# Optimization experiments

Measured on AMD Instinct MI355X. Metric: run time of the kernel, lower is better.

The kernel has to match this reference:

```python
import jax, jax.numpy as jnp
import numpy as np

B, N, DIM = 4, 2048, 3
H = 128          # hidden
K = 32           # num_neighbours
L = 4            # num_layers
OUT = 6          # out_per_particle


def _dense_init(key, fan_in, fan_out):
    kw, kb = jax.random.split(key)
    w = jax.random.normal(kw, (fan_in, fan_out), jnp.float32) / np.sqrt(fan_in)
    b = jnp.zeros((fan_out,), jnp.float32)
    return w, b


def setup_inputs() -> dict:
    key = jax.random.key(0)
    ks = jax.random.split(key, 8)
    x = jax.random.normal(ks[0], (B, N, DIM), jnp.float32)
    embed_w, embed_b = _dense_init(ks[1], DIM, H)
    # per-layer stacked params
    miw, mib, mow, mob, uiw, uib, uow, uob = [], [], [], [], [], [], [], []
    for l in range(L):
        k0, k1, k2, k3 = jax.random.split(jax.random.fold_in(ks[2], l), 4)
        w, b = _dense_init(k0, 2 * H + 1, H); miw.append(w); mib.append(b)
        w, b = _dense_init(k1, H, H);         mow.append(w); mob.append(b)
        w, b = _dense_init(k2, 2 * H, H);     uiw.append(w); uib.append(b)
        w, b = _dense_init(k3, H, H);         uow.append(w); uob.append(b)
    out_w, out_b = _dense_init(ks[3], H, OUT)
    return {
        'x': x,
        'embed_w': embed_w, 'embed_b': embed_b,
        'msg_in_w': jnp.stack(miw), 'msg_in_b': jnp.stack(mib),
        'msg_out_w': jnp.stack(mow), 'msg_out_b': jnp.stack(mob),
        'upd_in_w': jnp.stack(uiw), 'upd_in_b': jnp.stack(uib),
        'upd_out_w': jnp.stack(uow), 'upd_out_b': jnp.stack(uob),
        'out_w': out_w, 'out_b': out_b,
    }


def reference(x, embed_w, embed_b,
              msg_in_w, msg_in_b, msg_out_w, msg_out_b,
              upd_in_w, upd_in_b, upd_out_w, upd_out_b,
              out_w, out_b):
    act = jax.nn.silu
    n = x.shape[-2]
    # per-particle embed: (B,N,H)
    h = x @ embed_w + embed_b
    # pairwise squared distances (B,N,N), plain Euclidean (geometry=None)
    diff = x[..., :, None, :] - x[..., None, :, :]
    d_sq = jnp.sum(diff * diff, axis=-1)
    eye = jnp.eye(n, dtype=bool)
    d_sq = jnp.where(eye, jnp.inf, d_sq)
    neg_topk, idx_topk = jax.lax.top_k(-d_sq, K)      # (B,N,K)
    d_nearest = jnp.sqrt(jnp.maximum(-neg_topk, 0.0))  # (B,N,K)

    gather = jax.vmap(lambda hb, ib: hb[ib])  # (N,H),(N,K)->(N,K,H) over batch
    n_layers = msg_in_w.shape[0]
    for l in range(n_layers):
        nb = gather(h, idx_topk)                               # (B,N,K,H)
        node_i = jnp.broadcast_to(h[..., :, None, :], nb.shape)
        msg_inp = jnp.concatenate([node_i, nb, d_nearest[..., None]], axis=-1)
        msg = act(msg_inp @ msg_in_w[l] + msg_in_b[l]) @ msg_out_w[l] + msg_out_b[l]
        agg = jnp.sum(msg, axis=-2)                            # (B,N,H)
        upd_inp = jnp.concatenate([h, agg], axis=-1)
        upd = act(upd_inp @ upd_in_w[l] + upd_in_b[l]) @ upd_out_w[l] + upd_out_b[l]
        h = h + upd
    return h @ out_w + out_b
```

## Files before the change

kernel.cpp:

```cpp
#include <hip/hip_runtime.h>
#include <math.h>

#define B_ 4
#define N_ 2048
#define H_ 128
#define K_ 32
#define L_ 4
#define OUT_ 6
#define BN_ (B_*N_)
#define NPB_L 16
#define LBLK 512

typedef __attribute__((ext_vector_type(8))) short short8;
typedef __attribute__((ext_vector_type(4))) float f32x4;

#define LDW (H_ + 8)
#define LAYER_W 98304
#define OFF_W1A 0
#define OFF_W1C 16384
#define OFF_W2  32768
#define OFF_U1  49152
#define OFF_U2  81920
#define SCAP 256
#define KNN_ROWS 4
#define KNN_BLKS (BN_/KNN_ROWS)
#define PREP_BLKS (L_*LAYER_W/256)

#define LOG2E 1.44269504088896340736f
#define LN2   0.69314718055994530942f

__device__ __forceinline__ float silu_f(float x) {
    return __fdividef(x, 1.0f + __expf(-x));
}
__device__ __forceinline__ float silu_y(float y) {
    return __fdividef(y, 1.0f + __builtin_amdgcn_exp2f(-y));
}
__device__ __forceinline__ short f2b(float f) {
    unsigned u = __float_as_uint(f);
    return (short)((u + 0x7FFFu + ((u >> 16) & 1u)) >> 16);
}
__device__ __forceinline__ float b2f(short s) {
    return __uint_as_float(((unsigned)(unsigned short)s) << 16);
}
__device__ __forceinline__ unsigned pack2(short lo, short hi) {
    return (unsigned)(unsigned short)lo | ((unsigned)(unsigned short)hi << 16);
}
__device__ __forceinline__ int mbcnt64(unsigned long long m) {
    return __builtin_amdgcn_mbcnt_hi((unsigned)(m >> 32),
           __builtin_amdgcn_mbcnt_lo((unsigned)m, 0));
}

__global__ __launch_bounds__(256) void k_front(
    const float* __restrict__ x, int* __restrict__ nidx, float* __restrict__ ndist,
    const float* __restrict__ miw, const float* __restrict__ mow,
    const float* __restrict__ uiw, const float* __restrict__ uow,
    short* __restrict__ wt,
    const float* __restrict__ ew, const float* __restrict__ eb,
    const float* __restrict__ mib, float* __restrict__ Epack)
{
    __shared__ float xsx[N_], xsy[N_], xsz[N_];
    __shared__ unsigned skey[KNN_ROWS][SCAP];
    __shared__ int      sid [KNN_ROWS][SCAP];

    if (blockIdx.x >= KNN_BLKS + PREP_BLKS) {
        int t = threadIdx.x;
        int which = t >> 7, n = t & 127;
        const float* W = miw + (size_t)(which ? 128 : 0) * H_;
        float E0 = 0.f, E1 = 0.f, E2 = 0.f, Eb = 0.f;
        for (int k = 0; k < 128; ++k) {
            float w = W[(size_t)k*H_ + n];
            E0 = fmaf(ew[k],       w, E0);
            E1 = fmaf(ew[128 + k], w, E1);
            E2 = fmaf(ew[256 + k], w, E2);
            Eb = fmaf(eb[k],       w, Eb);
        }
        float* dst = Epack + which * 512;
        dst[0*128 + n] = E0 * LOG2E;
        dst[1*128 + n] = E1 * LOG2E;
        dst[2*128 + n] = E2 * LOG2E;
        dst[3*128 + n] = (Eb + (which ? 0.f : mib[n])) * LOG2E;
        return;
    }
    if (blockIdx.x >= KNN_BLKS) {
        int gid = (blockIdx.x - KNN_BLKS) * 256 + threadIdx.x;
        int l = gid / LAYER_W, o = gid - l * LAYER_W;
        float v;
        if (o < OFF_W1C) {
            int n = o >> 7, k = o & 127;
            v = miw[(size_t)l*257*H_ + k*H_ + n] * LOG2E;
        } else if (o < OFF_W2) {
            int oo = o - OFF_W1C, n = oo >> 7, k = oo & 127;
            v = miw[(size_t)l*257*H_ + (128 + k)*H_ + n] * LOG2E;
        } else if (o < OFF_U1) {
            int oo = o - OFF_W2, n = oo >> 7, k = oo & 127;
            v = mow[(size_t)l*H_*H_ + k*H_ + n];
        } else if (o < OFF_U2) {
            int oo = o - OFF_U1, n = oo >> 8, k = oo & 255;
            v = uiw[(size_t)l*2*H_*H_ + k*H_ + n];
        } else {
            int oo = o - OFF_U2, n = oo >> 7, k = oo & 127;
            v = uow[(size_t)l*H_*H_ + k*H_ + n];
        }
        wt[gid] = f2b(v);
        return;
    }

    int b  = blockIdx.x / (N_/KNN_ROWS);
    int i0 = (blockIdx.x % (N_/KNN_ROWS)) * KNN_ROWS;
    const float* xb = x + (size_t)b*N_*3;
    for (int t = threadIdx.x; t < N_*3; t += 256) {
        float v = xb[t];
        int q = t / 3, r = t - q*3;
        float* dst = (r == 0) ? xsx : (r == 1) ? xsy : xsz;
        dst[q] = v;
    }
    __syncthreads();

    int wave = threadIdx.x >> 6, lane = threadIdx.x & 63;
    int i = i0 + wave;
    float xix = xsx[i], xiy = xsy[i], xiz = xsz[i];

    unsigned u[N_/64];
    unsigned lmin = 0xFFFFFFFFu;
#pragma unroll
    for (int t = 0; t < N_/64; ++t) {
        int j = lane + 64*t;
        float d0 = xix-xsx[j], d1 = xiy-xsy[j], d2 = xiz-xsz[j];
        float d = d0*d0 + d1*d1 + d2*d2;
        unsigned k = (j == i) ? 0x7F800000u : __float_as_uint(d);
        u[t] = k;
        lmin = min(lmin, k);
    }
    unsigned mn = lmin, mx = lmin;
    for (int off = 32; off; off >>= 1) {
        unsigned o1 = (unsigned)__shfl_xor((int)mn, off); mn = min(mn, o1);
        unsigned o2 = (unsigned)__shfl_xor((int)mx, off); mx = max(mx, o2);
    }
    unsigned Tup = mn;
    if (mn != mx) {
        int hb = 31 - __clz((int)(mn ^ mx));
        Tup = mn & ~((2u << hb) - 1u);
        for (int bit = hb; bit >= 0; --bit) {
            unsigned cand = Tup | (1u << bit);
            if (__popcll(__ballot(lmin < cand)) < K_) Tup = cand;
        }
    }
    unsigned* sk = skey[wave];
    int*      si = sid [wave];
    int base = 0;
#pragma unroll
    for (int t = 0; t < N_/64; ++t) {
        bool pr = (u[t] <= Tup);
        unsigned long long m = __ballot(pr);
        if (pr) {
            int pos = base + mbcnt64(m);
            if (pos < SCAP) { sk[pos] = u[t]; si[pos] = lane + 64*t; }
        }
        base += __popcll(m);
    }
    int c = min(base, SCAP);
    unsigned sv[4]; int iv[4];
#pragma unroll
    for (int q = 0; q < 4; ++q) {
        int slot = lane + 64*q;
        bool ok = slot < c;
        sv[q] = ok ? sk[slot] : 0xFFFFFFFFu;
        iv[q] = ok ? si[slot] : 0;
    }
    unsigned T = mn;
    if (mn != Tup) {
        int hb = 31 - __clz((int)(mn ^ Tup));
        T = mn & ~((2u << hb) - 1u);
        for (int bit = hb; bit >= 0; --bit) {
            unsigned cand = T | (1u << bit);
            int cnt = __popcll(__ballot(sv[0] < cand)) + __popcll(__ballot(sv[1] < cand))
                    + __popcll(__ballot(sv[2] < cand)) + __popcll(__ballot(sv[3] < cand));
            if (cnt < K_) T = cand;
        }
    }
    int cnt_lt = __popcll(__ballot(sv[0] < T)) + __popcll(__ballot(sv[1] < T))
               + __popcll(__ballot(sv[2] < T)) + __popcll(__ballot(sv[3] < T));
    int need = K_ - cnt_lt;
    size_t rbase = ((size_t)(b*N_ + i)) * K_;
    int ltc = 0, eqc = 0;
#pragma unroll
    for (int q = 0; q < 4; ++q) {
        bool lt = sv[q] < T, eq = sv[q] == T;
        unsigned long long mlt = __ballot(lt), meq = __ballot(eq);
        int pp = ltc + mbcnt64(mlt), ee = eqc + mbcnt64(meq);
        ltc += __popcll(mlt); eqc += __popcll(meq);
        int pos = lt ? pp : ((eq && ee < need) ? (cnt_lt + ee) : -1);
        if (pos >= 0) {
            nidx [rbase + pos] = iv[q];
            ndist[rbase + pos] = sqrtf(__uint_as_float(sv[q]));
        }
    }
}

__global__ __launch_bounds__(512) void k_prep0(
    float* __restrict__ h, short* __restrict__ a, short* __restrict__ c0,
    const float* __restrict__ x, const float* __restrict__ ew,
    const float* __restrict__ eb, const float* __restrict__ Epack)
{
    int t = blockIdx.x * 512 + threadIdx.x;
    int node = t >> 7, ch = t & 127;
    const float* xp = x + (size_t)node*3;
    float x0 = xp[0], x1 = xp[1], x2 = xp[2];
    float hv = eb[ch];
    hv = fmaf(x0, ew[ch],       hv);
    hv = fmaf(x1, ew[H_+ch],    hv);
    hv = fmaf(x2, ew[2*H_+ch],  hv);
    float av = Epack[384+ch];
    av = fmaf(x0, Epack[ch],     av);
    av = fmaf(x1, Epack[128+ch], av);
    av = fmaf(x2, Epack[256+ch], av);
    float cv = Epack[896+ch];
    cv = fmaf(x0, Epack[512+ch], cv);
    cv = fmaf(x1, Epack[640+ch], cv);
    cv = fmaf(x2, Epack[768+ch], cv);
    size_t gi = (size_t)node*H_ + ch;
    h[gi]  = hv;
    a[gi]  = f2b(av);
    c0[gi] = f2b(cv);
}

__global__ __launch_bounds__(LBLK, 4) void k_layer(
    float* __restrict__ h, short* __restrict__ a,
    const int* __restrict__ nidx, const float* __restrict__ ndist,
    const float* __restrict__ wd,
    const short* __restrict__ wl,
    const float* __restrict__ b2, const float* __restrict__ u1b,
    const float* __restrict__ u2b,
    const short* __restrict__ c_rd, short* __restrict__ c_wr,
    const short* __restrict__ wn, const float* __restrict__ b1n, int do_ac,
    const float* __restrict__ ow, const float* __restrict__ ob,
    float* __restrict__ out)
{
    __shared__ __align__(16) short s_l[NPB_L][LDW];
    __shared__ __align__(16) short h_l[NPB_L][LDW];
    __shared__ __align__(16) short agg_l[NPB_L][LDW];
    __shared__ __align__(16) float h32s[NPB_L][H_];
    __shared__ int   idx_s[NPB_L][K_];
    __shared__ float dst_s[NPB_L][K_];
    int blk = blockIdx.x;
    int batch = (blk & 7) >> 1;
    int sub   = ((blk >> 3) << 1) | (blk & 1);
    int node0 = batch * N_ + sub * NPB_L;
    int tid = threadIdx.x;
    int wave = tid >> 6, lane = tid & 63, l15 = lane & 15, quad = lane >> 4;
    int ncol = wave*16 + l15;

    {
        float4 v = reinterpret_cast<const float4*>(h + (size_t)node0*H_)[tid];
        int row = tid >> 5, col = (tid & 31) * 4;
        h_l[row][col+0] = f2b(v.x); h_l[row][col+1] = f2b(v.y);
        h_l[row][col+2] = f2b(v.z); h_l[row][col+3] = f2b(v.w);
        *(float4*)&h32s[row][col] = v;
    }
    idx_s[tid>>5][tid&31] = nidx[(size_t)node0*K_ + tid];
    dst_s[tid>>5][tid&31] = ndist[(size_t)node0*K_ + tid];
    __syncthreads();

    short8 bw2[4];
#pragma unroll
    for (int kk = 0; kk < 4; ++kk)
        bw2[kk] = *(const short8*)(wl + OFF_W2 + (size_t)ncol*H_ + kk*32 + quad*8);

    {
        float wd0 = wd[2*lane] * LOG2E, wd1 = wd[2*lane+1] * LOG2E;
        int wavu = __builtin_amdgcn_readfirstlane(wave);
        const unsigned* c2 = (const unsigned*)c_rd + (size_t)batch*N_*(H_/2);
        const unsigned* a2 = (const unsigned*)a;
        int m0 = wavu*2, m1 = wavu*2 + 1;
        unsigned av0 = a2[(size_t)(node0+m0)*(H_/2) + lane];
        unsigned av1 = a2[(size_t)(node0+m1)*(H_/2) + lane];
        unsigned cv0[K_], cv1[K_];
#pragma unroll
        for (int k = 0; k < K_; ++k) {
            int j = __builtin_amdgcn_readfirstlane(idx_s[m0][k]);
            cv0[k] = c2[(size_t)j*(H_/2) + lane];
        }
#pragma unroll
        for (int k = 0; k < K_; ++k) {
            int j = __builtin_amdgcn_readfirstlane(idx_s[m1][k]);
            cv1[k] = c2[(size_t)j*(H_/2) + lane];
        }
        {
            float a0 = __uint_as_float(av0 << 16);
            float a1 = __uint_as_float(av0 & 0xFFFF0000u);
            float s0 = 0.f, s1 = 0.f;
#pragma unroll
            for (int k = 0; k < K_; ++k) {
                float dd = dst_s[m0][k];
                s0 += silu_y(a0 + fmaf(dd, wd0, __uint_as_float(cv0[k] << 16)));
                s1 += silu_y(a1 + fmaf(dd, wd1, __uint_as_float(cv0[k] & 0xFFFF0000u)));
            }
            *(unsigned*)&s_l[m0][2*lane] = pack2(f2b(s0 * LN2), f2b(s1 * LN2));
        }
        {
            float a0 = __uint_as_float(av1 << 16);
            float a1 = __uint_as_float(av1 & 0xFFFF0000u);
            float s0 = 0.f, s1 = 0.f;
#pragma unroll
            for (int k = 0; k < K_; ++k) {
                float dd = dst_s[m1][k];
                s0 += silu_y(a0 + fmaf(dd, wd0, __uint_as_float(cv1[k] << 16)));
                s1 += silu_y(a1 + fmaf(dd, wd1, __uint_as_float(cv1[k] & 0xFFFF0000u)));
            }
            *(unsigned*)&s_l[m1][2*lane] = pack2(f2b(s0 * LN2), f2b(s1 * LN2));
        }
    }
    short8 bu1[8], bu2[4];
#pragma unroll
    for (int kk = 0; kk < 8; ++kk)
        bu1[kk] = *(const short8*)(wl + OFF_U1 + (size_t)ncol*2*H_ + kk*32 + quad*8);
#pragma unroll
    for (int kk = 0; kk < 4; ++kk)
        bu2[kk] = *(const short8*)(wl + OFF_U2 + (size_t)ncol*H_ + kk*32 + quad*8);
    __syncthreads();

    f32x4 acc;
    acc = (f32x4){0,0,0,0};
#pragma unroll
    for (int kk = 0; kk < 4; ++kk) {
        int k0 = kk*32 + quad*8;
        short8 af = *(const short8*)&s_l[l15][k0];
        acc = __builtin_amdgcn_mfma_f32_16x16x32_bf16(af, bw2[kk], acc, 0, 0, 0);
    }
    {
        float b2v = b2[ncol] * (float)K_;
#pragma unroll
        for (int r = 0; r < 4; ++r)
            agg_l[quad*4 + r][ncol] = f2b(acc[r] + b2v);
    }
    __syncthreads();

    acc = (f32x4){0,0,0,0};
#pragma unroll
    for (int kk = 0; kk < 8; ++kk) {
        const short (*src)[LDW] = (kk < 4) ? h_l : agg_l;
        int kloc = ((kk < 4) ? kk*32 : (kk-4)*32) + quad*8;
        short8 af = *(const short8*)&src[l15][kloc];
        acc = __builtin_amdgcn_mfma_f32_16x16x32_bf16(af, bu1[kk], acc, 0, 0, 0);
    }
    short8 bacA[4], bacC[4];
    if (do_ac) {
#pragma unroll
        for (int kk = 0; kk < 4; ++kk) {
            bacA[kk] = *(const short8*)(wn + OFF_W1A + (size_t)ncol*H_ + kk*32 + quad*8);
            bacC[kk] = *(const short8*)(wn + OFF_W1C + (size_t)ncol*H_ + kk*32 + quad*8);
        }
    }
    {
        float u1bv = u1b[ncol];
#pragma unroll
        for (int r = 0; r < 4; ++r)
            s_l[quad*4 + r][ncol] = f2b(silu_f(acc[r] + u1bv));
    }
    __syncthreads();

    acc = (f32x4){0,0,0,0};
#pragma unroll
    for (int kk = 0; kk < 4; ++kk) {
        int k0 = kk*32 + quad*8;
        short8 af = *(const short8*)&s_l[l15][k0];
        acc = __builtin_amdgcn_mfma_f32_16x16x32_bf16(af, bu2[kk], acc, 0, 0, 0);
    }
    {
        float u2bv = u2b[ncol];
#pragma unroll
        for (int r = 0; r < 4; ++r) {
            int m = quad*4 + r;
            float nh = h32s[m][ncol] + acc[r] + u2bv;
            h[(size_t)(node0+m)*H_ + ncol] = nh;
            if (do_ac) h_l[m][ncol] = f2b(nh);
            else       h32s[m][ncol] = nh;
        }
    }
    if (do_ac) {
        __syncthreads();
        int n = ncol;
        f32x4 accA = (f32x4){0,0,0,0}, accC = (f32x4){0,0,0,0};
#pragma unroll
        for (int kk = 0; kk < 4; ++kk) {
            int k0 = kk*32 + quad*8;
            short8 af = *(const short8*)&h_l[l15][k0];
            accA = __builtin_amdgcn_mfma_f32_16x16x32_bf16(af, bacA[kk], accA, 0, 0, 0);
            accC = __builtin_amdgcn_mfma_f32_16x16x32_bf16(af, bacC[kk], accC, 0, 0, 0);
        }
        float b1v = b1n[n] * LOG2E;
#pragma unroll
        for (int r = 0; r < 4; ++r) {
            int m = quad*4 + r;
            size_t gi = (size_t)(node0+m)*H_ + n;
            a[gi]    = f2b(accA[r] + b1v);
            c_wr[gi] = f2b(accC[r]);
        }
    } else {
        __syncthreads();
        int node = tid >> 5, s = tid & 31;
        float p0=0.f,p1=0.f,p2=0.f,p3=0.f,p4=0.f,p5=0.f;
#pragma unroll
        for (int q = 0; q < 4; ++q) {
            int r = s + q*32;
            float hv = h32s[node][r];
            const float* owr = ow + r*OUT_;
            p0 = fmaf(hv, owr[0], p0); p1 = fmaf(hv, owr[1], p1);
            p2 = fmaf(hv, owr[2], p2); p3 = fmaf(hv, owr[3], p3);
            p4 = fmaf(hv, owr[4], p4); p5 = fmaf(hv, owr[5], p5);
        }
#pragma unroll
        for (int off = 16; off; off >>= 1) {
            p0 += __shfl_xor(p0, off); p1 += __shfl_xor(p1, off);
            p2 += __shfl_xor(p2, off); p3 += __shfl_xor(p3, off);
            p4 += __shfl_xor(p4, off); p5 += __shfl_xor(p5, off);
        }
        if (s == 0) {
            float* op = out + (size_t)(node0+node)*OUT_;
            op[0] = p0 + ob[0]; op[1] = p1 + ob[1]; op[2] = p2 + ob[2];
            op[3] = p3 + ob[3]; op[4] = p4 + ob[4]; op[5] = p5 + ob[5];
        }
    }
}

extern "C" void kernel_launch(void* const* d_in, const int* in_sizes, int n_in,
                              void* d_out, int out_size, void* d_ws, size_t ws_size,
                              hipStream_t stream)
{
    const float* x   = (const float*)d_in[0];
    const float* ew  = (const float*)d_in[1];
    const float* eb  = (const float*)d_in[2];
    const float* miw = (const float*)d_in[3];
    const float* mib = (const float*)d_in[4];
    const float* mow = (const float*)d_in[5];
    const float* mob = (const float*)d_in[6];
    const float* uiw = (const float*)d_in[7];
    const float* uib = (const float*)d_in[8];
    const float* uow = (const float*)d_in[9];
    const float* uob = (const float*)d_in[10];
    const float* ow  = (const float*)d_in[11];
    const float* ob  = (const float*)d_in[12];
    float* out = (float*)d_out;

    char* w = (char*)d_ws;
    float* h  = (float*)w;                         w += (size_t)BN_*H_*4;
    float* nd = (float*)w;                         w += (size_t)BN_*K_*4;
    int*   ni = (int*)w;                           w += (size_t)BN_*K_*4;
    short* a  = (short*)w;                         w += (size_t)BN_*H_*2;
    short* c0 = (short*)w;                         w += (size_t)BN_*H_*2;
    short* c1 = (short*)w;                         w += (size_t)BN_*H_*2;
    short* wt = (short*)w;                         w += (size_t)L_*LAYER_W*2;
    float* Epack = (float*)w;

    k_front<<<KNN_BLKS + PREP_BLKS + 1, 256, 0, stream>>>(x, ni, nd,
        miw, mow, uiw, uow, wt, ew, eb, mib, Epack);
    k_prep0<<<BN_*H_/512, 512, 0, stream>>>(h, a, c0, x, ew, eb, Epack);
    for (int l = 0; l < L_; ++l) {
        const short* c_rd = (l & 1) ? c1 : c0;
        short*       c_wr = (l & 1) ? c0 : c1;
        int do_ac = (l + 1 < L_);
        const short* wn = wt + (size_t)(do_ac ? (l+1) : l) * LAYER_W;
        const float* b1n = mib + (size_t)(do_ac ? (l+1) : l) * H_;
        k_layer<<<BN_/NPB_L, LBLK, 0, stream>>>(h, a, ni, nd,
            miw + (size_t)l*257*H_ + 256*H_,
            wt + (size_t)l*LAYER_W,
            mob + (size_t)l*H_, uib + (size_t)l*H_, uob + (size_t)l*H_,
            c_rd, c_wr, wn, b1n, do_ac,
            ow, ob, out);
    }
}
```

Baseline: 224.8 us.

## Fuse prep and per-layer kernels into one persistent kernel with grid barriers

Result: slower. 403.3 us (+79.4%).

```diff
diff --git a/kernel.cpp b/kernel.cpp
--- a/kernel.cpp
+++ b/kernel.cpp
@@ -10,6 +10,7 @@
 #define BN_ (B_*N_)
 #define NPB_L 16
 #define LBLK 512
+#define MAIN_BLKS (BN_/NPB_L)
 
 typedef __attribute__((ext_vector_type(8))) short short8;
 typedef __attribute__((ext_vector_type(4))) float f32x4;
@@ -39,15 +40,23 @@
     unsigned u = __float_as_uint(f);
     return (short)((u + 0x7FFFu + ((u >> 16) & 1u)) >> 16);
 }
-__device__ __forceinline__ float b2f(short s) {
-    return __uint_as_float(((unsigned)(unsigned short)s) << 16);
-}
 __device__ __forceinline__ unsigned pack2(short lo, short hi) {
     return (unsigned)(unsigned short)lo | ((unsigned)(unsigned short)hi << 16);
 }
 __device__ __forceinline__ int mbcnt64(unsigned long long m) {
     return __builtin_amdgcn_mbcnt_hi((unsigned)(m >> 32),
            __builtin_amdgcn_mbcnt_lo((unsigned)m, 0));
+}
+
+__device__ __forceinline__ void grid_bar_inv(unsigned* bar, unsigned nblk) {
+    __syncthreads();
+    if (threadIdx.x == 0) {
+        __hip_atomic_fetch_add(bar, 1u, __ATOMIC_RELAXED, __HIP_MEMORY_SCOPE_AGENT);
+        while (__hip_atomic_load(bar, __ATOMIC_RELAXED, __HIP_MEMORY_SCOPE_AGENT) < nblk)
+            __builtin_amdgcn_s_sleep(2);
+    }
+    __syncthreads();
+    asm volatile("buffer_inv sc0 sc1\n\ts_waitcnt vmcnt(0)" ::: "memory");
 }
 
 __global__ __launch_bounds__(256) void k_front(
@@ -56,7 +65,8 @@
     const float* __restrict__ uiw, const float* __restrict__ uow,
     short* __restrict__ wt,
     const float* __restrict__ ew, const float* __restrict__ eb,
-    const float* __restrict__ mib, float* __restrict__ Epack)
+    const float* __restrict__ mib, float* __restrict__ Epack,
+    unsigned* __restrict__ gbar)
 {
     __shared__ float xsx[N_], xsy[N_], xsz[N_];
     __shared__ unsigned skey[KNN_ROWS][SCAP];
@@ -64,6 +74,7 @@
 
     if (blockIdx.x >= KNN_BLKS + PREP_BLKS) {
         int t = threadIdx.x;
+        if (t < 4) gbar[t] = 0u;
         int which = t >> 7, n = t & 127;
         const float* W = miw + (size_t)(which ? 128 : 0) * H_;
         float E0 = 0.f, E1 = 0.f, E2 = 0.f, Eb = 0.f;
@@ -197,49 +208,22 @@
     }
 }
 
-__global__ __launch_bounds__(512) void k_prep0(
-    float* __restrict__ h, short* __restrict__ a, short* __restrict__ c0,
-    const float* __restrict__ x, const float* __restrict__ ew,
-    const float* __restrict__ eb, const float* __restrict__ Epack)
-{
-    int t = blockIdx.x * 512 + threadIdx.x;
-    int node = t >> 7, ch = t & 127;
-    const float* xp = x + (size_t)node*3;
-    float x0 = xp[0], x1 = xp[1], x2 = xp[2];
-    float hv = eb[ch];
-    hv = fmaf(x0, ew[ch],       hv);
-    hv = fmaf(x1, ew[H_+ch],    hv);
-    hv = fmaf(x2, ew[2*H_+ch],  hv);
-    float av = Epack[384+ch];
-    av = fmaf(x0, Epack[ch],     av);
-    av = fmaf(x1, Epack[128+ch], av);
-    av = fmaf(x2, Epack[256+ch], av);
-    float cv = Epack[896+ch];
-    cv = fmaf(x0, Epack[512+ch], cv);
-    cv = fmaf(x1, Epack[640+ch], cv);
-    cv = fmaf(x2, Epack[768+ch], cv);
-    size_t gi = (size_t)node*H_ + ch;
-    h[gi]  = hv;
-    a[gi]  = f2b(av);
-    c0[gi] = f2b(cv);
-}
-
-__global__ __launch_bounds__(LBLK, 4) void k_layer(
-    float* __restrict__ h, short* __restrict__ a,
+__global__ __launch_bounds__(LBLK, 4) void k_main(
     const int* __restrict__ nidx, const float* __restrict__ ndist,
-    const float* __restrict__ wd,
-    const short* __restrict__ wl,
-    const float* __restrict__ b2, const float* __restrict__ u1b,
-    const float* __restrict__ u2b,
-    const short* __restrict__ c_rd, short* __restrict__ c_wr,
-    const short* __restrict__ wn, const float* __restrict__ b1n, int do_ac,
+    const float* __restrict__ miw, const short* __restrict__ wt,
+    const float* __restrict__ mob, const float* __restrict__ uib,
+    const float* __restrict__ uob, const float* __restrict__ mib,
+    short* __restrict__ c0buf, short* __restrict__ c1buf,
+    const float* __restrict__ x, const float* __restrict__ Epack,
+    const float* __restrict__ ew, const float* __restrict__ eb,
     const float* __restrict__ ow, const float* __restrict__ ob,
-    float* __restrict__ out)
+    float* __restrict__ out, unsigned* __restrict__ gbar)
 {
     __shared__ __align__(16) short s_l[NPB_L][LDW];
     __shared__ __align__(16) short h_l[NPB_L][LDW];
     __shared__ __align__(16) short agg_l[NPB_L][LDW];
     __shared__ __align__(16) float h32s[NPB_L][H_];
+    __shared__ __align__(16) short a_l[NPB_L][H_];
     __shared__ int   idx_s[NPB_L][K_];
     __shared__ float dst_s[NPB_L][K_];
     int blk = blockIdx.x;
@@ -250,154 +234,200 @@
     int wave = tid >> 6, lane = tid & 63, l15 = lane & 15, quad = lane >> 4;
     int ncol = wave*16 + l15;
 
-    {
-        float4 v = reinterpret_cast<const float4*>(h + (size_t)node0*H_)[tid];
-        int row = tid >> 5, col = (tid & 31) * 4;
-        h_l[row][col+0] = f2b(v.x); h_l[row][col+1] = f2b(v.y);
-        h_l[row][col+2] = f2b(v.z); h_l[row][col+3] = f2b(v.w);
-        *(float4*)&h32s[row][col] = v;
-    }
     idx_s[tid>>5][tid&31] = nidx[(size_t)node0*K_ + tid];
     dst_s[tid>>5][tid&31] = ndist[(size_t)node0*K_ + tid];
-    __syncthreads();
-
-    short8 bw2[4];
-#pragma unroll
-    for (int kk = 0; kk < 4; ++kk)
-        bw2[kk] = *(const short8*)(wl + OFF_W2 + (size_t)ncol*H_ + kk*32 + quad*8);
 
     {
-        float wd0 = wd[2*lane] * LOG2E, wd1 = wd[2*lane+1] * LOG2E;
-        int wavu = __builtin_amdgcn_readfirstlane(wave);
-        const unsigned* c2 = (const unsigned*)c_rd + (size_t)batch*N_*(H_/2);
-        const unsigned* a2 = (const unsigned*)a;
-        int m0 = wavu*2, m1 = wavu*2 + 1;
-        unsigned av0 = a2[(size_t)(node0+m0)*(H_/2) + lane];
-        unsigned av1 = a2[(size_t)(node0+m1)*(H_/2) + lane];
-        unsigned cv0[K_], cv1[K_];
-#pragma unroll
-        for (int k = 0; k < K_; ++k) {
-            int j = __builtin_amdgcn_readfirstlane(idx_s[m0][k]);
-            cv0[k] = c2[(size_t)j*(H_/2) + lane];
-        }
-#pragma unroll
-        for (int k = 0; k < K_; ++k) {
-            int j = __builtin_amdgcn_readfirstlane(idx_s[m1][k]);
-            cv1[k] = c2[(size_t)j*(H_/2) + lane];
-        }
+        unsigned* c0w = (unsigned*)c0buf;
+        for (int t = tid; t < NPB_L*(H_/2); t += LBLK) {
+            int node = t >> 6, cp = t & 63;
+            int ch0 = 2*cp, ch1 = 2*cp + 1;
+            int gr = node0 + node;
+            const float* xp = x + (size_t)gr*3;
+            float x0 = xp[0], x1 = xp[1], x2 = xp[2];
+            float h0 = eb[ch0];
+            h0 = fmaf(x0, ew[ch0],      h0);
+            h0 = fmaf(x1, ew[H_+ch0],   h0);
+            h0 = fmaf(x2, ew[2*H_+ch0], h0);
+            float h1 = eb[ch1];
+            h1 = fmaf(x0, ew[ch1],      h1);
+            h1 = fmaf(x1, ew[H_+ch1],   h1);
+            h1 = fmaf(x2, ew[2*H_+ch1], h1);
+            float a0 = Epack[384+ch0];
+            a0 = fmaf(x0, Epack[ch0],     a0);
+            a0 = fmaf(x1, Epack[128+ch0], a0);
+            a0 = fmaf(x2, Epack[256+ch0], a0);
+            float a1 = Epack[384+ch1];
+            a1 = fmaf(x0, Epack[ch1],     a1);
+            a1 = fmaf(x1, Epack[128+ch1], a1);
+            a1 = fmaf(x2, Epack[256+ch1], a1);
+            float c0v = Epack[896+ch0];
+            c0v = fmaf(x0, Epack[512+ch0], c0v);
+            c0v = fmaf(x1, Epack[640+ch0], c0v);
+            c0v = fmaf(x2, Epack[768+ch0], c0v);
+            float c1v = Epack[896+ch1];
+            c1v = fmaf(x0, Epack[512+ch1], c1v);
+            c1v = fmaf(x1, Epack[640+ch1], c1v);
+            c1v = fmaf(x2, Epack[768+ch1], c1v);
+            h32s[node][ch0] = h0;  h32s[node][ch1] = h1;
+            h_l[node][ch0] = f2b(h0);  h_l[node][ch1] = f2b(h1);
+            a_l[node][ch0] = f2b(a0);  a_l[node][ch1] = f2b(a1);
+            __hip_atomic_store(&c0w[(size_t)gr*(H_/2) + cp],
+                               pack2(f2b(c0v), f2b(c1v)),
+                               __ATOMIC_RELAXED, __HIP_MEMORY_SCOPE_AGENT);
+        }
+    }
+    grid_bar_inv(gbar + 0, MAIN_BLKS);
+
+    for (int l = 0; l < L_; ++l) {
+        int do_ac = (l + 1 < L_);
+        const short* wl  = wt  + (size_t)l * LAYER_W;
+        const float* wd  = miw + (size_t)l*257*H_ + 256*H_;
+        const short* c_rd = (l & 1) ? c1buf : c0buf;
+        short*       c_wr = (l & 1) ? c0buf : c1buf;
+        const float* b2  = mob + (size_t)l*H_;
+        const float* u1b = uib + (size_t)l*H_;
+        const float* u2b = uob + (size_t)l*H_;
+        const short* wn  = wt  + (size_t)(l+1) * LAYER_W;
+        const float* b1n = mib + (size_t)(l+1) * H_;
+
+        short8 bw2[4], bu1[8], bu2[4];
+#pragma unroll
+        for (int kk = 0; kk < 4; ++kk)
+            bw2[kk] = *(const short8*)(wl + OFF_W2 + (size_t)ncol*H_ + kk*32 + quad*8);
+#pragma unroll
+        for (int kk = 0; kk < 8; ++kk)
+            bu1[kk] = *(const short8*)(wl + OFF_U1 + (size_t)ncol*2*H_ + kk*32 + quad*8);
+#pragma unroll
+        for (int kk = 0; kk < 4; ++kk)
+            bu2[kk] = *(const short8*)(wl + OFF_U2 + (size_t)ncol*H_ + kk*32 + quad*8);
+
         {
-            float a0 = __uint_as_float(av0 << 16);
-            float a1 = __uint_as_float(av0 & 0xFFFF0000u);
-            float s0 = 0.f, s1 = 0.f;
-#pragma unroll
-            for (int k = 0; k < K_; ++k) {
-                float dd = dst_s[m0][k];
-                s0 += silu_y(a0 + fmaf(dd, wd0, __uint_as_float(cv0[k] << 16)));
-                s1 += silu_y(a1 + fmaf(dd, wd1, __uint_as_float(cv0[k] & 0xFFFF0000u)));
+            float wd0 = wd[2*lane] * LOG2E, wd1 = wd[2*lane+1] * LOG2E;
+            int wavu = __builtin_amdgcn_readfirstlane(wave);
+            const unsigned* c2 = (const unsigned*)c_rd + (size_t)batch*N_*(H_/2);
+#pragma unroll
+            for (int nn = 0; nn < 2; ++nn) {
+                int m = wavu*2 + nn;
+                unsigned av = *(const unsigned*)&a_l[m][2*lane];
+                float a0 = __uint_as_float(av << 16);
+                float a1 = __uint_as_float(av & 0xFFFF0000u);
+                unsigned cva[16], cvb[16];
+#pragma unroll
+                for (int k = 0; k < 16; ++k) {
+                    int j = __builtin_amdgcn_readfirstlane(idx_s[m][k]);
+                    cva[k] = c2[(size_t)j*(H_/2) + lane];
+                }
+#pragma unroll
+                for (int k = 0; k < 16; ++k) {
+                    int j = __builtin_amdgcn_readfirstlane(idx_s[m][16+k]);
+                    cvb[k] = c2[(size_t)j*(H_/2) + lane];
+                }
+                float s0 = 0.f, s1 = 0.f;
+#pragma unroll
+                for (int k = 0; k < 16; ++k) {
+                    float dd = dst_s[m][k];
+                    s0 += silu_y(a0 + fmaf(dd, wd0, __uint_as_float(cva[k] << 16)));
+                    s1 += silu_y(a1 + fmaf(dd, wd1, __uint_as_float(cva[k] & 0xFFFF0000u)));
+                }
+#pragma unroll
+                for (int k = 0; k < 16; ++k) {
+                    float dd = dst_s[m][16+k];
+                    s0 += silu_y(a0 + fmaf(dd, wd0, __uint_as_float(cvb[k] << 16)));
+                    s1 += silu_y(a1 + fmaf(dd, wd1, __uint_as_float(cvb[k] & 0xFFFF0000u)));
+                }
+                *(unsigned*)&s_l[m][2*lane] = pack2(f2b(s0 * LN2), f2b(s1 * LN2));
             }
-            *(unsigned*)&s_l[m0][2*lane] = pack2(f2b(s0 * LN2), f2b(s1 * LN2));
-        }
-        {
-            float a0 = __uint_as_float(av1 << 16);
-            float a1 = __uint_as_float(av1 & 0xFFFF0000u);
-            float s0 = 0.f, s1 = 0.f;
-#pragma unroll
-            for (int k = 0; k < K_; ++k) {
-                float dd = dst_s[m1][k];
-                s0 += silu_y(a0 + fmaf(dd, wd0, __uint_as_float(cv1[k] << 16)));
-                s1 += silu_y(a1 + fmaf(dd, wd1, __uint_as_float(cv1[k] & 0xFFFF0000u)));
-            }
-            *(unsigned*)&s_l[m1][2*lane] = pack2(f2b(s0 * LN2), f2b(s1 * LN2));
-        }
-    }
-    short8 bu1[8], bu2[4];
-#pragma unroll
-    for (int kk = 0; kk < 8; ++kk)
-        bu1[kk] = *(const short8*)(wl + OFF_U1 + (size_t)ncol*2*H_ + kk*32 + quad*8);
-#pragma unroll
-    for (int kk = 0; kk < 4; ++kk)
-        bu2[kk] = *(const short8*)(wl + OFF_U2 + (size_t)ncol*H_ + kk*32 + quad*8);
-    __syncthreads();
-
-    f32x4 acc;
-    acc = (f32x4){0,0,0,0};
-#pragma unroll
-    for (int kk = 0; kk < 4; ++kk) {
-        int k0 = kk*32 + quad*8;
-        short8 af = *(const short8*)&s_l[l15][k0];
-        acc = __builtin_amdgcn_mfma_f32_16x16x32_bf16(af, bw2[kk], acc, 0, 0, 0);
-    }
-    {
-        float b2v = b2[ncol] * (float)K_;
-#pragma unroll
-        for (int r = 0; r < 4; ++r)
-            agg_l[quad*4 + r][ncol] = f2b(acc[r] + b2v);
-    }
-    __syncthreads();
-
-    acc = (f32x4){0,0,0,0};
-#pragma unroll
-    for (int kk = 0; kk < 8; ++kk) {
-        const short (*src)[LDW] = (kk < 4) ? h_l : agg_l;
-        int kloc = ((kk < 4) ? kk*32 : (kk-4)*32) + quad*8;
-        short8 af = *(const short8*)&src[l15][kloc];
-        acc = __builtin_amdgcn_mfma_f32_16x16x32_bf16(af, bu1[kk], acc, 0, 0, 0);
-    }
-    short8 bacA[4], bacC[4];
-    if (do_ac) {
-#pragma unroll
-        for (int kk = 0; kk < 4; ++kk) {
-            bacA[kk] = *(const short8*)(wn + OFF_W1A + (size_t)ncol*H_ + kk*32 + quad*8);
-            bacC[kk] = *(const short8*)(wn + OFF_W1C + (size_t)ncol*H_ + kk*32 + quad*8);
-        }
-    }
-    {
-        float u1bv = u1b[ncol];
-#pragma unroll
-        for (int r = 0; r < 4; ++r)
-            s_l[quad*4 + r][ncol] = f2b(silu_f(acc[r] + u1bv));
-    }
-    __syncthreads();
-
-    acc = (f32x4){0,0,0,0};
-#pragma unroll
-    for (int kk = 0; kk < 4; ++kk) {
-        int k0 = kk*32 + quad*8;
-        short8 af = *(const short8*)&s_l[l15][k0];
-        acc = __builtin_amdgcn_mfma_f32_16x16x32_bf16(af, bu2[kk], acc, 0, 0, 0);
-    }
-    {
-        float u2bv = u2b[ncol];
-#pragma unroll
-        for (int r = 0; r < 4; ++r) {
-            int m = quad*4 + r;
-            float nh = h32s[m][ncol] + acc[r] + u2bv;
-            h[(size_t)(node0+m)*H_ + ncol] = nh;
-            if (do_ac) h_l[m][ncol] = f2b(nh);
-            else       h32s[m][ncol] = nh;
-        }
-    }
-    if (do_ac) {
+        }
         __syncthreads();
-        int n = ncol;
-        f32x4 accA = (f32x4){0,0,0,0}, accC = (f32x4){0,0,0,0};
+
+        f32x4 acc;
+        acc = (f32x4){0,0,0,0};
 #pragma unroll
         for (int kk = 0; kk < 4; ++kk) {
             int k0 = kk*32 + quad*8;
-            short8 af = *(const short8*)&h_l[l15][k0];
-            accA = __builtin_amdgcn_mfma_f32_16x16x32_bf16(af, bacA[kk], accA, 0, 0, 0);
-            accC = __builtin_amdgcn_mfma_f32_16x16x32_bf16(af, bacC[kk], accC, 0, 0, 0);
-        }
-        float b1v = b1n[n] * LOG2E;
-#pragma unroll
-        for (int r = 0; r < 4; ++r) {
-            int m = quad*4 + r;
-            size_t gi = (size_t)(node0+m)*H_ + n;
-            a[gi]    = f2b(accA[r] + b1v);
-            c_wr[gi] = f2b(accC[r]);
-        }
-    } else {
+            short8 af = *(const short8*)&s_l[l15][k0];
+            acc = __builtin_amdgcn_mfma_f32_16x16x32_bf16(af, bw2[kk], acc, 0, 0, 0);
+        }
+        {
+            float b2v = b2[ncol] * (float)K_;
+#pragma unroll
+            for (int r = 0; r < 4; ++r)
+                agg_l[quad*4 + r][ncol] = f2b(acc[r] + b2v);
+        }
         __syncthreads();
+
+        acc = (f32x4){0,0,0,0};
+#pragma unroll
+        for (int kk = 0; kk < 8; ++kk) {
+            const short (*src)[LDW] = (kk < 4) ? h_l : agg_l;
+            int kloc = ((kk < 4) ? kk*32 : (kk-4)*32) + quad*8;
+            short8 af = *(const short8*)&src[l15][kloc];
+            acc = __builtin_amdgcn_mfma_f32_16x16x32_bf16(af, bu1[kk], acc, 0, 0, 0);
+        }
+        short8 bacA[4], bacC[4];
+        if (do_ac) {
+#pragma unroll
+            for (int kk = 0; kk < 4; ++kk) {
+                bacA[kk] = *(const short8*)(wn + OFF_W1A + (size_t)ncol*H_ + kk*32 + quad*8);
+                bacC[kk] = *(const short8*)(wn + OFF_W1C + (size_t)ncol*H_ + kk*32 + quad*8);
+            }
+        }
+        {
+            float u1bv = u1b[ncol];
+#pragma unroll
+            for (int r = 0; r < 4; ++r)
+                s_l[quad*4 + r][ncol] = f2b(silu_f(acc[r] + u1bv));
+        }
+        __syncthreads();
+
+        acc = (f32x4){0,0,0,0};
+#pragma unroll
+        for (int kk = 0; kk < 4; ++kk) {
+            int k0 = kk*32 + quad*8;
+            short8 af = *(const short8*)&s_l[l15][k0];
+            acc = __builtin_amdgcn_mfma_f32_16x16x32_bf16(af, bu2[kk], acc, 0, 0, 0);
+        }
+        {
+            float u2bv = u2b[ncol];
+#pragma unroll
+            for (int r = 0; r < 4; ++r) {
+                int m = quad*4 + r;
+                float nh = h32s[m][ncol] + acc[r] + u2bv;
+                h32s[m][ncol] = nh;
+                if (do_ac) h_l[m][ncol] = f2b(nh);
+            }
+        }
+        if (do_ac) {
+            __syncthreads();
+            int n = ncol;
+            f32x4 accA = (f32x4){0,0,0,0}, accC = (f32x4){0,0,0,0};
+#pragma unroll
+            for (int kk = 0; kk < 4; ++kk) {
+                int k0 = kk*32 + quad*8;
+                short8 af = *(const short8*)&h_l[l15][k0];
+                accA = __builtin_amdgcn_mfma_f32_16x16x32_bf16(af, bacA[kk], accA, 0, 0, 0);
+                accC = __builtin_amdgcn_mfma_f32_16x16x32_bf16(af, bacC[kk], accC, 0, 0, 0);
+            }
+            float b1v = b1n[n] * LOG2E;
+            unsigned* c2w = (unsigned*)c_wr;
+#pragma unroll
+            for (int r = 0; r < 4; ++r) {
+                int m = quad*4 + r;
+                a_l[m][n] = f2b(accA[r] + b1v);
+                float oc = __shfl_xor(accC[r], 1);
+                if (!(lane & 1)) {
+                    unsigned pk = pack2(f2b(accC[r]), f2b(oc));
+                    __hip_atomic_store(&c2w[(size_t)(node0+m)*(H_/2) + (n >> 1)], pk,
+                                       __ATOMIC_RELAXED, __HIP_MEMORY_SCOPE_AGENT);
+                }
+            }
+            grid_bar_inv(gbar + 1 + l, MAIN_BLKS);
+        }
+    }
+
+    __syncthreads();
+    {
         int node = tid >> 5, s = tid & 31;
         float p0=0.f,p1=0.f,p2=0.f,p3=0.f,p4=0.f,p5=0.f;
 #pragma unroll
@@ -443,29 +473,18 @@
     float* out = (float*)d_out;
 
     char* w = (char*)d_ws;
-    float* h  = (float*)w;                         w += (size_t)BN_*H_*4;
     float* nd = (float*)w;                         w += (size_t)BN_*K_*4;
     int*   ni = (int*)w;                           w += (size_t)BN_*K_*4;
-    short* a  = (short*)w;                         w += (size_t)BN_*H_*2;
     short* c0 = (short*)w;                         w += (size_t)BN_*H_*2;
     short* c1 = (short*)w;                         w += (size_t)BN_*H_*2;
     short* wt = (short*)w;                         w += (size_t)L_*LAYER_W*2;
-    float* Epack = (float*)w;
+    float* Epack = (float*)w;                      w += (size_t)1024*4;
+    unsigned* gbar = (unsigned*)w;
 
     k_front<<<KNN_BLKS + PREP_BLKS + 1, 256, 0, stream>>>(x, ni, nd,
-        miw, mow, uiw, uow, wt, ew, eb, mib, Epack);
-    k_prep0<<<BN_*H_/512, 512, 0, stream>>>(h, a, c0, x, ew, eb, Epack);
-    for (int l = 0; l < L_; ++l) {
-        const short* c_rd = (l & 1) ? c1 : c0;
-        short*       c_wr = (l & 1) ? c0 : c1;
-        int do_ac = (l + 1 < L_);
-        const short* wn = wt + (size_t)(do_ac ? (l+1) : l) * LAYER_W;
-        const float* b1n = mib + (size_t)(do_ac ? (l+1) : l) * H_;
-        k_layer<<<BN_/NPB_L, LBLK, 0, stream>>>(h, a, ni, nd,
-            miw + (size_t)l*257*H_ + 256*H_,
-            wt + (size_t)l*LAYER_W,
-            mob + (size_t)l*H_, uib + (size_t)l*H_, uob + (size_t)l*H_,
-            c_rd, c_wr, wn, b1n, do_ac,
-            ow, ob, out);
-    }
-}
+        miw, mow, uiw, uow, wt, ew, eb, mib, Epack, gbar);
+    k_main<<<MAIN_BLKS, LBLK, 0, stream>>>(ni, nd,
+        miw, wt, mob, uib, uob, mib,
+        c0, c1, x, Epack, ew, eb,
+        ow, ob, out, gbar);
+}
```

## Cut register pressure in layer kernel by chunking neighbour gathers and deferring weight loads

Applied to the files above, without the earlier changes.

New measurement: 202.7 us. -9.8%, faster.

```diff
diff --git a/kernel.cpp b/kernel.cpp
--- a/kernel.cpp
+++ b/kernel.cpp
@@ -30,17 +30,12 @@
 #define LN2   0.69314718055994530942f
 
 __device__ __forceinline__ float silu_f(float x) {
-    return __fdividef(x, 1.0f + __expf(-x));
-}
-__device__ __forceinline__ float silu_y(float y) {
-    return __fdividef(y, 1.0f + __builtin_amdgcn_exp2f(-y));
+    float e = __builtin_amdgcn_exp2f(-x * LOG2E);
+    return x * __builtin_amdgcn_rcpf(1.0f + e);
 }
 __device__ __forceinline__ short f2b(float f) {
     unsigned u = __float_as_uint(f);
     return (short)((u + 0x7FFFu + ((u >> 16) & 1u)) >> 16);
-}
-__device__ __forceinline__ float b2f(short s) {
-    return __uint_as_float(((unsigned)(unsigned short)s) << 16);
 }
 __device__ __forceinline__ unsigned pack2(short lo, short hi) {
     return (unsigned)(unsigned short)lo | ((unsigned)(unsigned short)hi << 16);
@@ -261,62 +256,38 @@
     dst_s[tid>>5][tid&31] = ndist[(size_t)node0*K_ + tid];
     __syncthreads();
 
-    short8 bw2[4];
-#pragma unroll
-    for (int kk = 0; kk < 4; ++kk)
-        bw2[kk] = *(const short8*)(wl + OFF_W2 + (size_t)ncol*H_ + kk*32 + quad*8);
-
     {
         float wd0 = wd[2*lane] * LOG2E, wd1 = wd[2*lane+1] * LOG2E;
         int wavu = __builtin_amdgcn_readfirstlane(wave);
         const unsigned* c2 = (const unsigned*)c_rd + (size_t)batch*N_*(H_/2);
         const unsigned* a2 = (const unsigned*)a;
-        int m0 = wavu*2, m1 = wavu*2 + 1;
-        unsigned av0 = a2[(size_t)(node0+m0)*(H_/2) + lane];
-        unsigned av1 = a2[(size_t)(node0+m1)*(H_/2) + lane];
-        unsigned cv0[K_], cv1[K_];
-#pragma unroll
-        for (int k = 0; k < K_; ++k) {
-            int j = __builtin_amdgcn_readfirstlane(idx_s[m0][k]);
-            cv0[k] = c2[(size_t)j*(H_/2) + lane];
-        }
-#pragma unroll
-        for (int k = 0; k < K_; ++k) {
-            int j = __builtin_amdgcn_readfirstlane(idx_s[m1][k]);
-            cv1[k] = c2[(size_t)j*(H_/2) + lane];
-        }
-        {
-            float a0 = __uint_as_float(av0 << 16);
-            float a1 = __uint_as_float(av0 & 0xFFFF0000u);
+        for (int nn = 0; nn < 2; ++nn) {
+            int m = wavu*2 + nn;
+            unsigned av = a2[(size_t)(node0+m)*(H_/2) + lane];
+            float a0 = __uint_as_float(av << 16);
+            float a1 = __uint_as_float(av & 0xFFFF0000u);
             float s0 = 0.f, s1 = 0.f;
-#pragma unroll
-            for (int k = 0; k < K_; ++k) {
-                float dd = dst_s[m0][k];
-                s0 += silu_y(a0 + fmaf(dd, wd0, __uint_as_float(cv0[k] << 16)));
-                s1 += silu_y(a1 + fmaf(dd, wd1, __uint_as_float(cv0[k] & 0xFFFF0000u)));
+            for (int kc = 0; kc < K_; kc += 8) {
+                unsigned cv[8];
+#pragma unroll
+                for (int k = 0; k < 8; ++k) {
+                    int j = __builtin_amdgcn_readfirstlane(idx_s[m][kc + k]);
+                    cv[k] = c2[(size_t)j*(H_/2) + lane];
+                }
+#pragma unroll
+                for (int k = 0; k < 8; ++k) {
+                    float dd = dst_s[m][kc + k];
+                    float y0 = a0 + fmaf(dd, wd0, __uint_as_float(cv[k] << 16));
+                    float y1 = a1 + fmaf(dd, wd1, __uint_as_float(cv[k] & 0xFFFF0000u));
+                    float t0 = __builtin_amdgcn_rcpf(1.0f + __builtin_amdgcn_exp2f(-y0));
+                    float t1 = __builtin_amdgcn_rcpf(1.0f + __builtin_amdgcn_exp2f(-y1));
+                    s0 = fmaf(y0, t0, s0);
+                    s1 = fmaf(y1, t1, s1);
+                }
             }
-            *(unsigned*)&s_l[m0][2*lane] = pack2(f2b(s0 * LN2), f2b(s1 * LN2));
-        }
-        {
-            float a0 = __uint_as_float(av1 << 16);
-            float a1 = __uint_as_float(av1 & 0xFFFF0000u);
-            float s0 = 0.f, s1 = 0.f;
-#pragma unroll
-            for (int k = 0; k < K_; ++k) {
-                float dd = dst_s[m1][k];
-                s0 += silu_y(a0 + fmaf(dd, wd0, __uint_as_float(cv1[k] << 16)));
-                s1 += silu_y(a1 + fmaf(dd, wd1, __uint_as_float(cv1[k] & 0xFFFF0000u)));
-            }
-            *(unsigned*)&s_l[m1][2*lane] = pack2(f2b(s0 * LN2), f2b(s1 * LN2));
-        }
-    }
-    short8 bu1[8], bu2[4];
-#pragma unroll
-    for (int kk = 0; kk < 8; ++kk)
-        bu1[kk] = *(const short8*)(wl + OFF_U1 + (size_t)ncol*2*H_ + kk*32 + quad*8);
-#pragma unroll
-    for (int kk = 0; kk < 4; ++kk)
-        bu2[kk] = *(const short8*)(wl + OFF_U2 + (size_t)ncol*H_ + kk*32 + quad*8);
+            *(unsigned*)&s_l[m][2*lane] = pack2(f2b(s0 * LN2), f2b(s1 * LN2));
+        }
+    }
     __syncthreads();
 
     f32x4 acc;
@@ -324,8 +295,9 @@
 #pragma unroll
     for (int kk = 0; kk < 4; ++kk) {
         int k0 = kk*32 + quad*8;
+        short8 bf = *(const short8*)(wl + OFF_W2 + (size_t)ncol*H_ + k0);
         short8 af = *(const short8*)&s_l[l15][k0];
-        acc = __builtin_amdgcn_mfma_f32_16x16x32_bf16(af, bw2[kk], acc, 0, 0, 0);
+        acc = __builtin_amdgcn_mfma_f32_16x16x32_bf16(af, bf, acc, 0, 0, 0);
     }
     {
         float b2v = b2[ncol] * (float)K_;
@@ -340,16 +312,9 @@
     for (int kk = 0; kk < 8; ++kk) {
         const short (*src)[LDW] = (kk < 4) ? h_l : agg_l;
         int kloc = ((kk < 4) ? kk*32 : (kk-4)*32) + quad*8;
+        short8 bf = *(const short8*)(wl + OFF_U1 + (size_t)ncol*2*H_ + kk*32 + quad*8);
         short8 af = *(const short8*)&src[l15][kloc];
-        acc = __builtin_amdgcn_mfma_f32_16x16x32_bf16(af, bu1[kk], acc, 0, 0, 0);
-    }
-    short8 bacA[4], bacC[4];
-    if (do_ac) {
-#pragma unroll
-        for (int kk = 0; kk < 4; ++kk) {
-            bacA[kk] = *(const short8*)(wn + OFF_W1A + (size_t)ncol*H_ + kk*32 + quad*8);
-            bacC[kk] = *(const short8*)(wn + OFF_W1C + (size_t)ncol*H_ + kk*32 + quad*8);
-        }
+        acc = __builtin_amdgcn_mfma_f32_16x16x32_bf16(af, bf, acc, 0, 0, 0);
     }
     {
         float u1bv = u1b[ncol];
@@ -363,8 +328,9 @@
 #pragma unroll
     for (int kk = 0; kk < 4; ++kk) {
         int k0 = kk*32 + quad*8;
+        short8 bf = *(const short8*)(wl + OFF_U2 + (size_t)ncol*H_ + k0);
         short8 af = *(const short8*)&s_l[l15][k0];
-        acc = __builtin_amdgcn_mfma_f32_16x16x32_bf16(af, bu2[kk], acc, 0, 0, 0);
+        acc = __builtin_amdgcn_mfma_f32_16x16x32_bf16(af, bf, acc, 0, 0, 0);
     }
     {
         float u2bv = u2b[ncol];
@@ -385,8 +351,10 @@
         for (int kk = 0; kk < 4; ++kk) {
             int k0 = kk*32 + quad*8;
             short8 af = *(const short8*)&h_l[l15][k0];
-            accA = __builtin_amdgcn_mfma_f32_16x16x32_bf16(af, bacA[kk], accA, 0, 0, 0);
-            accC = __builtin_amdgcn_mfma_f32_16x16x32_bf16(af, bacC[kk], accC, 0, 0, 0);
+            short8 bA = *(const short8*)(wn + OFF_W1A + (size_t)ncol*H_ + k0);
+            short8 bC = *(const short8*)(wn + OFF_W1C + (size_t)ncol*H_ + k0);
+            accA = __builtin_amdgcn_mfma_f32_16x16x32_bf16(af, bA, accA, 0, 0, 0);
+            accC = __builtin_amdgcn_mfma_f32_16x16x32_bf16(af, bC, accC, 0, 0, 0);
         }
         float b1v = b1n[n] * LOG2E;
 #pragma unroll
```
